# Performance work log

Measured on AMD Instinct MI355X. Metric: run time of the kernel, lower is better.

## Reference

```python
import jax, jax.numpy as jnp
import numpy as np
from jax import lax

RES = 2048
MAX_VAL = 1.0
COST_SCALE = 0.01
N_ITERS = 10
BOUNDARY_FRAC = 0.02  # sparse scattered Dirichlet cells, realistic for a planner occupancy grid


def _neighbor_sum(V):
    # replicate-pad (zero-Neumann at the outer border), 4-point stencil sum
    Vp = jnp.pad(V, 1, mode='edge')
    return Vp[:-2, 1:-1] + Vp[2:, 1:-1] + Vp[1:-1, :-2] + Vp[1:-1, 2:]


def setup_inputs() -> dict:
    key = jax.random.key(0)
    k1, k2, k3, k4 = jax.random.split(key, 4)
    x = jax.random.uniform(k1, (RES, RES), jnp.float32)
    # sparse boundary/obstacle cells (boundary_types > 0 means Dirichlet cell)
    boundary_types = (jax.random.uniform(k2, (RES, RES)) < BOUNDARY_FRAC).astype(jnp.int32)
    boundary_conditions = jax.random.uniform(k3, (RES, RES), jnp.float32)
    # learnable cost field, initialized around cost_scale (some negatives so ReLU matters)
    C = COST_SCALE + COST_SCALE * jax.random.normal(k4, (RES, RES), jnp.float32)
    return {'x': x, 'C': C, 'boundary_types': boundary_types,
            'boundary_conditions': boundary_conditions}


def reference(x, C, boundary_types, boundary_conditions):
    mask = boundary_types > 0
    # inject boundary conditions into the initial potential (x[obj_inds] = bc[obj_inds])
    V = jnp.where(mask, boundary_conditions, x)
    C_pos = jax.nn.relu(C)
    denom = 4.0 + C_pos  # screened Laplace: (4 + C) V = sum(neighbors)

    def step(V, _):
        V_new = _neighbor_sum(V) / denom
        V_new = jnp.where(mask, boundary_conditions, V_new)
        return V_new, None

    V, _ = lax.scan(step, V, None, length=N_ITERS)

    out = jnp.where(V >= MAX_VAL, 0.95 * MAX_VAL, V)
    out = jnp.where(mask, boundary_conditions, out)
    return out, C_pos
```

## Files before the change

kernel.cpp:

```cpp
#include <hip/hip_runtime.h>


#define RES    2048
#define HALO   10
#define DIMX   128
#define DIMY   56
#define OUTX   (DIMX - 2*HALO)
#define OUTY   (DIMY - 2*HALO)
#define NBX    ((RES + OUTX - 1) / OUTX)
#define NBY    ((RES + OUTY - 1) / OUTY)
#define NITER  10

__global__ __launch_bounds__(256, 2)
void laplace10_fused(const float* __restrict__ Xin,
                     const float* __restrict__ Cin,
                     const int*   __restrict__ BT,
                     const float* __restrict__ BCin,
                     float* __restrict__ OUT,
                     float* __restrict__ CPOS) {
  __shared__ __align__(16) float buf[2][DIMY][DIMX];
  float* const s0 = &buf[0][0][0];
  float* const s1 = &buf[1][0][0];

  const int t   = threadIdx.x;
  const int q   = t & 31;
  const int ty  = t >> 5;
  const int x0  = q * 4;
  const int y0  = ty * 7;
  const int tx0 = (int)blockIdx.x * OUTX - HALO;
  const int ty0 = (int)blockIdx.y * OUTY - HALO;
  const int gx0 = tx0 + x0;

  const bool xedge = (tx0 < 0) || (tx0 + DIMX > RES);

  auto stage = [&](const float* __restrict__ g, float* __restrict__ sb) {
    if (!xedge) {
#pragma unroll
      for (int i = 0; i < 14; ++i) {
        const int idx = t + i * 256;
        const int y   = idx >> 6;
        const int xx  = (idx & 63) * 2;
        int gy = ty0 + y;
        gy = gy < 0 ? 0 : (gy > RES - 1 ? RES - 1 : gy);
        *(float2*)(sb + y * DIMX + xx) =
            *(const float2*)(g + (size_t)gy * RES + (tx0 + xx));
      }
    } else {
#pragma unroll
      for (int i = 0; i < 14; ++i) {
        const int idx = t + i * 256;
        const int y   = idx >> 6;
        const int xx  = (idx & 63) * 2;
        int gy = ty0 + y;
        gy = gy < 0 ? 0 : (gy > RES - 1 ? RES - 1 : gy);
        int ga = tx0 + xx, gb = tx0 + xx + 1;
        ga = ga < 0 ? 0 : (ga > RES - 1 ? RES - 1 : ga);
        gb = gb < 0 ? 0 : (gb > RES - 1 ? RES - 1 : gb);
        float2 v;
        v.x = g[(size_t)gy * RES + ga];
        v.y = g[(size_t)gy * RES + gb];
        *(float2*)(sb + y * DIMX + xx) = v;
      }
    }
  };

  const bool in0 = (x0 + 0 >= HALO) && (x0 + 0 < HALO + OUTX);
  const bool in1 = (x0 + 1 >= HALO) && (x0 + 1 < HALO + OUTX);
  const bool in2 = (x0 + 2 >= HALO) && (x0 + 2 < HALO + OUTX);
  const bool in3 = (x0 + 3 >= HALO) && (x0 + 3 < HALO + OUTX);
  const bool fullq = in0 && in3 && (gx0 + 4 <= RES);

  stage((const float*)BT, s1);
  __syncthreads();
  unsigned mb = 0u;
#pragma unroll
  for (int i = 0; i < 7; ++i) {
    const float4 mv = *(const float4*)(s1 + (y0 + i) * DIMX + x0);
    if (__float_as_uint(mv.x) != 0u) mb |= 1u << (i * 4 + 0);
    if (__float_as_uint(mv.y) != 0u) mb |= 1u << (i * 4 + 1);
    if (__float_as_uint(mv.z) != 0u) mb |= 1u << (i * 4 + 2);
    if (__float_as_uint(mv.w) != 0u) mb |= 1u << (i * 4 + 3);
  }
  __syncthreads();

  stage(BCin, s1);
  __syncthreads();
  float4 Bq[7];
#pragma unroll
  for (int i = 0; i < 7; ++i) {
    const float4 b = *(const float4*)(s1 + (y0 + i) * DIMX + x0);
    Bq[i].x = (mb >> (i * 4 + 0) & 1u) ? b.x : 0.0f;
    Bq[i].y = (mb >> (i * 4 + 1) & 1u) ? b.y : 0.0f;
    Bq[i].z = (mb >> (i * 4 + 2) & 1u) ? b.z : 0.0f;
    Bq[i].w = (mb >> (i * 4 + 3) & 1u) ? b.w : 0.0f;
  }
  __syncthreads();

  stage(Cin, s1);
  __syncthreads();
  float4 Rq[7];
#pragma unroll
  for (int i = 0; i < 7; ++i) {
    const int y = y0 + i;
    const float4 c = *(const float4*)(s1 + y * DIMX + x0);
    float4 cp;
    cp.x = c.x > 0.0f ? c.x : 0.0f;
    cp.y = c.y > 0.0f ? c.y : 0.0f;
    cp.z = c.z > 0.0f ? c.z : 0.0f;
    cp.w = c.w > 0.0f ? c.w : 0.0f;
    Rq[i].x = (mb >> (i * 4 + 0) & 1u) ? 0.0f : 1.0f / (4.0f + cp.x);
    Rq[i].y = (mb >> (i * 4 + 1) & 1u) ? 0.0f : 1.0f / (4.0f + cp.y);
    Rq[i].z = (mb >> (i * 4 + 2) & 1u) ? 0.0f : 1.0f / (4.0f + cp.z);
    Rq[i].w = (mb >> (i * 4 + 3) & 1u) ? 0.0f : 1.0f / (4.0f + cp.w);
    const int gy = ty0 + y;
    if (y >= HALO && y < HALO + OUTY && gy < RES) {
      const size_t ro = (size_t)gy * RES;
      if (fullq) {
        *(float2*)(CPOS + ro + gx0)     = make_float2(cp.x, cp.y);
        *(float2*)(CPOS + ro + gx0 + 2) = make_float2(cp.z, cp.w);
      } else {
        if (in0 && gx0 + 0 < RES) CPOS[ro + gx0 + 0] = cp.x;
        if (in1 && gx0 + 1 < RES) CPOS[ro + gx0 + 1] = cp.y;
        if (in2 && gx0 + 2 < RES) CPOS[ro + gx0 + 2] = cp.z;
        if (in3 && gx0 + 3 < RES) CPOS[ro + gx0 + 3] = cp.w;
      }
    }
  }
  __syncthreads();

  stage(Xin, s1);
  __syncthreads();
#pragma unroll
  for (int i = 0; i < 7; ++i) {
    const float4 xv = *(const float4*)(s1 + (y0 + i) * DIMX + x0);
    float4 v0;
    v0.x = (mb >> (i * 4 + 0) & 1u) ? Bq[i].x : xv.x;
    v0.y = (mb >> (i * 4 + 1) & 1u) ? Bq[i].y : xv.y;
    v0.z = (mb >> (i * 4 + 2) & 1u) ? Bq[i].z : xv.z;
    v0.w = (mb >> (i * 4 + 3) & 1u) ? Bq[i].w : xv.w;
    *(float4*)(s0 + (y0 + i) * DIMX + x0) = v0;
  }
  __syncthreads();

  const int xm = (x0 == 0) ? 0 : x0 - 1;
  const int xp = (x0 + 4 >= DIMX) ? DIMX - 1 : x0 + 4;
  const bool lq0 = (gx0 + 0 <= 0);
  const bool lq1 = (gx0 + 1 <= 0);
  const bool lq2 = (gx0 + 2 <= 0);
  const bool lq3 = (gx0 + 3 <= 0);
  const bool rq0 = (gx0 + 0 >= RES - 1);
  const bool rq1 = (gx0 + 1 >= RES - 1);
  const bool rq2 = (gx0 + 2 >= RES - 1);
  const bool rq3 = (gx0 + 3 >= RES - 1);

#pragma unroll
  for (int it = 1; it <= NITER; ++it) {
    const float* const src = (it & 1) ? s0 : s1;
    float* const dst       = (it & 1) ? s1 : s0;
    float4 v[9];
#pragma unroll
    for (int j = 0; j < 9; ++j) {
      int r = y0 - 1 + j;
      r = r < 0 ? 0 : (r > DIMY - 1 ? DIMY - 1 : r);
      v[j] = *(const float4*)(src + r * DIMX + x0);
    }
#pragma unroll
    for (int i = 0; i < 7; ++i) {
      const int y = y0 + i;
      if (y < it || y >= DIMY - it) continue;
      const int gy = ty0 + y;
      const float lf = src[y * DIMX + xm];
      const float rt = src[y * DIMX + xp];
      const float4 vm = v[i + 1];
      const float4 va = (gy <= 0)       ? vm : v[i];
      const float4 vb = (gy >= RES - 1) ? vm : v[i + 2];
      const float n0 = va.x + vb.x + (lq0 ? vm.x : lf)   + (rq0 ? vm.x : vm.y);
      const float n1 = va.y + vb.y + (lq1 ? vm.y : vm.x) + (rq1 ? vm.y : vm.z);
      const float n2 = va.z + vb.z + (lq2 ? vm.z : vm.y) + (rq2 ? vm.z : vm.w);
      const float n3 = va.w + vb.w + (lq3 ? vm.w : vm.z) + (rq3 ? vm.w : rt);
      float4 nv;
      nv.x = fmaf(n0, Rq[i].x, Bq[i].x);
      nv.y = fmaf(n1, Rq[i].y, Bq[i].y);
      nv.z = fmaf(n2, Rq[i].z, Bq[i].z);
      nv.w = fmaf(n3, Rq[i].w, Bq[i].w);
      if (it < NITER) {
        *(float4*)(dst + y * DIMX + x0) = nv;
      } else {
        if (gy < RES) {
          const float o0 = (nv.x >= 1.0f) ? 0.95f : nv.x;
          const float o1 = (nv.y >= 1.0f) ? 0.95f : nv.y;
          const float o2 = (nv.z >= 1.0f) ? 0.95f : nv.z;
          const float o3 = (nv.w >= 1.0f) ? 0.95f : nv.w;
          const size_t ro = (size_t)gy * RES;
          if (fullq) {
            *(float2*)(OUT + ro + gx0)     = make_float2(o0, o1);
            *(float2*)(OUT + ro + gx0 + 2) = make_float2(o2, o3);
          } else {
            if (in0 && gx0 + 0 < RES) OUT[ro + gx0 + 0] = o0;
            if (in1 && gx0 + 1 < RES) OUT[ro + gx0 + 1] = o1;
            if (in2 && gx0 + 2 < RES) OUT[ro + gx0 + 2] = o2;
            if (in3 && gx0 + 3 < RES) OUT[ro + gx0 + 3] = o3;
          }
        }
      }
    }
    if (it < NITER) __syncthreads();
  }
}

extern "C" void kernel_launch(void* const* d_in, const int* in_sizes, int n_in,
                              void* d_out, int out_size, void* d_ws, size_t ws_size,
                              hipStream_t stream) {
  const float* Xin  = (const float*)d_in[0];
  const float* Cin  = (const float*)d_in[1];
  const int*   BT   = (const int*)d_in[2];
  const float* BCin = (const float*)d_in[3];
  float* OUT  = (float*)d_out;
  float* CPOS = OUT + (size_t)RES * RES;

  dim3 grid(NBX, NBY);
  dim3 block(256);
  hipLaunchKernelGGL(laplace10_fused, grid, block, 0, stream,
                     Xin, Cin, BT, BCin, OUT, CPOS);
}
```

Before: 152.0 us.

## Single-buffer LDS stencil with direct global loads, shuffles, and XCD-aware block remap

Replaces the double-buffered shared tile with one buffer updated in place between two barriers per iteration. Inputs are loaded straight from global memory into registers instead of being staged through shared memory. Left and right neighbours now come from wavefront shuffles rather than LDS reads. The launch becomes a 1D grid remapped so neighbouring tiles land on the same XCD, and the x halo grows to 12 so stores stay float4-aligned, with the occupancy hint raised to 4 blocks. Together these aim to cut LDS footprint and traffic and raise occupancy, at the cost of an extra barrier per iteration and more redundant halo work.

```diff
diff --git a/kernel.cpp b/kernel.cpp
--- a/kernel.cpp
+++ b/kernel.cpp
@@ -2,148 +2,53 @@
 
 
 #define RES    2048
-#define HALO   10
+#define XHALO  12
+#define YHALO  10
 #define DIMX   128
 #define DIMY   56
-#define OUTX   (DIMX - 2*HALO)
-#define OUTY   (DIMY - 2*HALO)
+#define OUTX   (DIMX - 2*XHALO)
+#define OUTY   (DIMY - 2*YHALO)
 #define NBX    ((RES + OUTX - 1) / OUTX)
 #define NBY    ((RES + OUTY - 1) / OUTY)
+#define NWG    (NBX*NBY)
 #define NITER  10
 
-__global__ __launch_bounds__(256, 2)
+__global__ __launch_bounds__(256, 4)
 void laplace10_fused(const float* __restrict__ Xin,
                      const float* __restrict__ Cin,
-                     const int*   __restrict__ BT,
+                     const float* __restrict__ BTf,
                      const float* __restrict__ BCin,
                      float* __restrict__ OUT,
                      float* __restrict__ CPOS) {
-  __shared__ __align__(16) float buf[2][DIMY][DIMX];
-  float* const s0 = &buf[0][0][0];
-  float* const s1 = &buf[1][0][0];
+  __shared__ __align__(16) float V[DIMY][DIMX];
 
-  const int t   = threadIdx.x;
-  const int q   = t & 31;
-  const int ty  = t >> 5;
-  const int x0  = q * 4;
-  const int y0  = ty * 7;
-  const int tx0 = (int)blockIdx.x * OUTX - HALO;
-  const int ty0 = (int)blockIdx.y * OUTY - HALO;
+  const int t  = threadIdx.x;
+  const int q  = t & 31;
+  const int ty = t >> 5;
+  const int x0 = q * 4;
+  const int y0 = ty * 7;
+
+  int wg = (int)blockIdx.x;
+  {
+    const int qq = NWG / 8, rr = NWG % 8;
+    const int xcd = wg % 8, off = wg / 8;
+    wg = (xcd < rr ? xcd * (qq + 1) : rr * (qq + 1) + (xcd - rr) * qq) + off;
+  }
+  const int bx  = wg % NBX, by = wg / NBX;
+  const int tx0 = bx * OUTX - XHALO;
+  const int ty0 = by * OUTY - YHALO;
   const int gx0 = tx0 + x0;
 
-  const bool xedge = (tx0 < 0) || (tx0 + DIMX > RES);
+  const bool xfull = (gx0 >= 0) && (gx0 + 4 <= RES);
+  const int  xcl   = (gx0 < 0) ? 0 : (RES - 1);
+  const bool xin   = (x0 >= XHALO) && (x0 < XHALO + OUTX) && xfull;
 
-  auto stage = [&](const float* __restrict__ g, float* __restrict__ sb) {
-    if (!xedge) {
-#pragma unroll
-      for (int i = 0; i < 14; ++i) {
-        const int idx = t + i * 256;
-        const int y   = idx >> 6;
-        const int xx  = (idx & 63) * 2;
-        int gy = ty0 + y;
-        gy = gy < 0 ? 0 : (gy > RES - 1 ? RES - 1 : gy);
-        *(float2*)(sb + y * DIMX + xx) =
-            *(const float2*)(g + (size_t)gy * RES + (tx0 + xx));
-      }
-    } else {
-#pragma unroll
-      for (int i = 0; i < 14; ++i) {
-        const int idx = t + i * 256;
-        const int y   = idx >> 6;
-        const int xx  = (idx & 63) * 2;
-        int gy = ty0 + y;
-        gy = gy < 0 ? 0 : (gy > RES - 1 ? RES - 1 : gy);
-        int ga = tx0 + xx, gb = tx0 + xx + 1;
-        ga = ga < 0 ? 0 : (ga > RES - 1 ? RES - 1 : ga);
-        gb = gb < 0 ? 0 : (gb > RES - 1 ? RES - 1 : gb);
-        float2 v;
-        v.x = g[(size_t)gy * RES + ga];
-        v.y = g[(size_t)gy * RES + gb];
-        *(float2*)(sb + y * DIMX + xx) = v;
-      }
-    }
+  auto load4 = [&](const float* __restrict__ g, int row) -> float4 {
+    if (xfull) return *(const float4*)(g + (size_t)row * RES + gx0);
+    const float v = g[(size_t)row * RES + xcl];
+    return make_float4(v, v, v, v);
   };
 
-  const bool in0 = (x0 + 0 >= HALO) && (x0 + 0 < HALO + OUTX);
-  const bool in1 = (x0 + 1 >= HALO) && (x0 + 1 < HALO + OUTX);
-  const bool in2 = (x0 + 2 >= HALO) && (x0 + 2 < HALO + OUTX);
-  const bool in3 = (x0 + 3 >= HALO) && (x0 + 3 < HALO + OUTX);
-  const bool fullq = in0 && in3 && (gx0 + 4 <= RES);
-
-  stage((const float*)BT, s1);
-  __syncthreads();
-  unsigned mb = 0u;
-#pragma unroll
-  for (int i = 0; i < 7; ++i) {
-    const float4 mv = *(const float4*)(s1 + (y0 + i) * DIMX + x0);
-    if (__float_as_uint(mv.x) != 0u) mb |= 1u << (i * 4 + 0);
-    if (__float_as_uint(mv.y) != 0u) mb |= 1u << (i * 4 + 1);
-    if (__float_as_uint(mv.z) != 0u) mb |= 1u << (i * 4 + 2);
-    if (__float_as_uint(mv.w) != 0u) mb |= 1u << (i * 4 + 3);
-  }
-  __syncthreads();
-
-  stage(BCin, s1);
-  __syncthreads();
-  float4 Bq[7];
-#pragma unroll
-  for (int i = 0; i < 7; ++i) {
-    const float4 b = *(const float4*)(s1 + (y0 + i) * DIMX + x0);
-    Bq[i].x = (mb >> (i * 4 + 0) & 1u) ? b.x : 0.0f;
-    Bq[i].y = (mb >> (i * 4 + 1) & 1u) ? b.y : 0.0f;
-    Bq[i].z = (mb >> (i * 4 + 2) & 1u) ? b.z : 0.0f;
-    Bq[i].w = (mb >> (i * 4 + 3) & 1u) ? b.w : 0.0f;
-  }
-  __syncthreads();
-
-  stage(Cin, s1);
-  __syncthreads();
-  float4 Rq[7];
-#pragma unroll
-  for (int i = 0; i < 7; ++i) {
-    const int y = y0 + i;
-    const float4 c = *(const float4*)(s1 + y * DIMX + x0);
-    float4 cp;
-    cp.x = c.x > 0.0f ? c.x : 0.0f;
-    cp.y = c.y > 0.0f ? c.y : 0.0f;
-    cp.z = c.z > 0.0f ? c.z : 0.0f;
-    cp.w = c.w > 0.0f ? c.w : 0.0f;
-    Rq[i].x = (mb >> (i * 4 + 0) & 1u) ? 0.0f : 1.0f / (4.0f + cp.x);
-    Rq[i].y = (mb >> (i * 4 + 1) & 1u) ? 0.0f : 1.0f / (4.0f + cp.y);
-    Rq[i].z = (mb >> (i * 4 + 2) & 1u) ? 0.0f : 1.0f / (4.0f + cp.z);
-    Rq[i].w = (mb >> (i * 4 + 3) & 1u) ? 0.0f : 1.0f / (4.0f + cp.w);
-    const int gy = ty0 + y;
-    if (y >= HALO && y < HALO + OUTY && gy < RES) {
-      const size_t ro = (size_t)gy * RES;
-      if (fullq) {
-        *(float2*)(CPOS + ro + gx0)     = make_float2(cp.x, cp.y);
-        *(float2*)(CPOS + ro + gx0 + 2) = make_float2(cp.z, cp.w);
-      } else {
-        if (in0 && gx0 + 0 < RES) CPOS[ro + gx0 + 0] = cp.x;
-        if (in1 && gx0 + 1 < RES) CPOS[ro + gx0 + 1] = cp.y;
-        if (in2 && gx0 + 2 < RES) CPOS[ro + gx0 + 2] = cp.z;
-        if (in3 && gx0 + 3 < RES) CPOS[ro + gx0 + 3] = cp.w;
-      }
-    }
-  }
-  __syncthreads();
-
-  stage(Xin, s1);
-  __syncthreads();
-#pragma unroll
-  for (int i = 0; i < 7; ++i) {
-    const float4 xv = *(const float4*)(s1 + (y0 + i) * DIMX + x0);
-    float4 v0;
-    v0.x = (mb >> (i * 4 + 0) & 1u) ? Bq[i].x : xv.x;
-    v0.y = (mb >> (i * 4 + 1) & 1u) ? Bq[i].y : xv.y;
-    v0.z = (mb >> (i * 4 + 2) & 1u) ? Bq[i].z : xv.z;
-    v0.w = (mb >> (i * 4 + 3) & 1u) ? Bq[i].w : xv.w;
-    *(float4*)(s0 + (y0 + i) * DIMX + x0) = v0;
-  }
-  __syncthreads();
-
-  const int xm = (x0 == 0) ? 0 : x0 - 1;
-  const int xp = (x0 + 4 >= DIMX) ? DIMX - 1 : x0 + 4;
   const bool lq0 = (gx0 + 0 <= 0);
   const bool lq1 = (gx0 + 1 <= 0);
   const bool lq2 = (gx0 + 2 <= 0);
@@ -153,58 +58,125 @@
   const bool rq2 = (gx0 + 2 >= RES - 1);
   const bool rq3 = (gx0 + 3 >= RES - 1);
 
+  unsigned mb = 0u;
+  float4 Bq[7], Rq[7];
 #pragma unroll
-  for (int it = 1; it <= NITER; ++it) {
-    const float* const src = (it & 1) ? s0 : s1;
-    float* const dst       = (it & 1) ? s1 : s0;
-    float4 v[9];
+  for (int i = 0; i < 7; ++i) {
+    const int gr  = ty0 + y0 + i;
+    const int gyc = gr < 0 ? 0 : (gr > RES - 1 ? RES - 1 : gr);
+    const float4 mv = load4(BTf, gyc);
+    const float4 bv = load4(BCin, gyc);
+    const unsigned m0 = (__float_as_uint(mv.x) != 0u);
+    const unsigned m1 = (__float_as_uint(mv.y) != 0u);
+    const unsigned m2 = (__float_as_uint(mv.z) != 0u);
+    const unsigned m3 = (__float_as_uint(mv.w) != 0u);
+    mb |= (m0 | (m1 << 1) | (m2 << 2) | (m3 << 3)) << (4 * i);
+    Bq[i].x = m0 ? bv.x : 0.0f;
+    Bq[i].y = m1 ? bv.y : 0.0f;
+    Bq[i].z = m2 ? bv.z : 0.0f;
+    Bq[i].w = m3 ? bv.w : 0.0f;
+  }
 #pragma unroll
-    for (int j = 0; j < 9; ++j) {
-      int r = y0 - 1 + j;
-      r = r < 0 ? 0 : (r > DIMY - 1 ? DIMY - 1 : r);
-      v[j] = *(const float4*)(src + r * DIMX + x0);
+  for (int i = 0; i < 7; ++i) {
+    const int gr  = ty0 + y0 + i;
+    const int gyc = gr < 0 ? 0 : (gr > RES - 1 ? RES - 1 : gr);
+    const float4 c = load4(Cin, gyc);
+    float4 cp;
+    cp.x = c.x > 0.0f ? c.x : 0.0f;
+    cp.y = c.y > 0.0f ? c.y : 0.0f;
+    cp.z = c.z > 0.0f ? c.z : 0.0f;
+    cp.w = c.w > 0.0f ? c.w : 0.0f;
+    Rq[i].x = (mb >> (4 * i + 0) & 1u) ? 0.0f : 1.0f / (4.0f + cp.x);
+    Rq[i].y = (mb >> (4 * i + 1) & 1u) ? 0.0f : 1.0f / (4.0f + cp.y);
+    Rq[i].z = (mb >> (4 * i + 2) & 1u) ? 0.0f : 1.0f / (4.0f + cp.z);
+    Rq[i].w = (mb >> (4 * i + 3) & 1u) ? 0.0f : 1.0f / (4.0f + cp.w);
+    const int yy = y0 + i;
+    if (xin && yy >= YHALO && yy < YHALO + OUTY && gr >= 0 && gr < RES) {
+      *(float4*)(CPOS + (size_t)gr * RES + gx0) = cp;
     }
+  }
+#pragma unroll
+  for (int i = 0; i < 7; ++i) {
+    const int gr  = ty0 + y0 + i;
+    const int gyc = gr < 0 ? 0 : (gr > RES - 1 ? RES - 1 : gr);
+    const float4 xv = load4(Xin, gyc);
+    float4 v0;
+    v0.x = (mb >> (4 * i + 0) & 1u) ? Bq[i].x : xv.x;
+    v0.y = (mb >> (4 * i + 1) & 1u) ? Bq[i].y : xv.y;
+    v0.z = (mb >> (4 * i + 2) & 1u) ? Bq[i].z : xv.z;
+    v0.w = (mb >> (4 * i + 3) & 1u) ? Bq[i].w : xv.w;
+    *(float4*)(&V[y0 + i][x0]) = v0;
+  }
+  __syncthreads();
+
+  auto compute_ns = [&](float4* ns) {
+    const int ym1 = (y0 == 0) ? 0 : y0 - 1;
+    float4 ra = *(const float4*)(&V[ym1][x0]);
+    float4 rb = *(const float4*)(&V[y0][x0]);
 #pragma unroll
     for (int i = 0; i < 7; ++i) {
-      const int y = y0 + i;
-      if (y < it || y >= DIMY - it) continue;
-      const int gy = ty0 + y;
-      const float lf = src[y * DIMX + xm];
-      const float rt = src[y * DIMX + xp];
-      const float4 vm = v[i + 1];
-      const float4 va = (gy <= 0)       ? vm : v[i];
-      const float4 vb = (gy >= RES - 1) ? vm : v[i + 2];
-      const float n0 = va.x + vb.x + (lq0 ? vm.x : lf)   + (rq0 ? vm.x : vm.y);
-      const float n1 = va.y + vb.y + (lq1 ? vm.y : vm.x) + (rq1 ? vm.y : vm.z);
-      const float n2 = va.z + vb.z + (lq2 ? vm.z : vm.y) + (rq2 ? vm.z : vm.w);
-      const float n3 = va.w + vb.w + (lq3 ? vm.w : vm.z) + (rq3 ? vm.w : rt);
-      float4 nv;
-      nv.x = fmaf(n0, Rq[i].x, Bq[i].x);
-      nv.y = fmaf(n1, Rq[i].y, Bq[i].y);
-      nv.z = fmaf(n2, Rq[i].z, Bq[i].z);
-      nv.w = fmaf(n3, Rq[i].w, Bq[i].w);
-      if (it < NITER) {
-        *(float4*)(dst + y * DIMX + x0) = nv;
-      } else {
-        if (gy < RES) {
-          const float o0 = (nv.x >= 1.0f) ? 0.95f : nv.x;
-          const float o1 = (nv.y >= 1.0f) ? 0.95f : nv.y;
-          const float o2 = (nv.z >= 1.0f) ? 0.95f : nv.z;
-          const float o3 = (nv.w >= 1.0f) ? 0.95f : nv.w;
-          const size_t ro = (size_t)gy * RES;
-          if (fullq) {
-            *(float2*)(OUT + ro + gx0)     = make_float2(o0, o1);
-            *(float2*)(OUT + ro + gx0 + 2) = make_float2(o2, o3);
-          } else {
-            if (in0 && gx0 + 0 < RES) OUT[ro + gx0 + 0] = o0;
-            if (in1 && gx0 + 1 < RES) OUT[ro + gx0 + 1] = o1;
-            if (in2 && gx0 + 2 < RES) OUT[ro + gx0 + 2] = o2;
-            if (in3 && gx0 + 3 < RES) OUT[ro + gx0 + 3] = o3;
-          }
+      const int yy = y0 + i;
+      const int yp = (yy >= DIMY - 1) ? (DIMY - 1) : (yy + 1);
+      const float4 rc = *(const float4*)(&V[yp][x0]);
+      const float lf = __shfl(rb.w, (t + 63) & 63);
+      const float rt = __shfl(rb.x, (t + 1) & 63);
+      const int g = ty0 + yy;
+      const float4 vm = rb;
+      const float4 va = (g <= 0) ? vm : ra;
+      const float4 vb = (g >= RES - 1) ? vm : rc;
+      float4 n;
+      n.x = va.x + vb.x + (lq0 ? vm.x : lf)   + (rq0 ? vm.x : vm.y);
+      n.y = va.y + vb.y + (lq1 ? vm.y : vm.x) + (rq1 ? vm.y : vm.z);
+      n.z = va.z + vb.z + (lq2 ? vm.z : vm.y) + (rq2 ? vm.z : vm.w);
+      n.w = va.w + vb.w + (lq3 ? vm.w : vm.z) + (rq3 ? vm.w : rt);
+      ns[i] = n;
+      ra = rb; rb = rc;
+    }
+  };
+
+#pragma unroll 1
+  for (int it = 1; it < NITER; ++it) {
+    float4 ns[7];
+    compute_ns(ns);
+    __syncthreads();
+#pragma unroll
+    for (int i = 0; i < 7; ++i) {
+      const int yy = y0 + i;
+      if (yy >= it && yy < DIMY - it) {
+        float4 nv;
+        nv.x = fmaf(ns[i].x, Rq[i].x, Bq[i].x);
+        nv.y = fmaf(ns[i].y, Rq[i].y, Bq[i].y);
+        nv.z = fmaf(ns[i].z, Rq[i].z, Bq[i].z);
+        nv.w = fmaf(ns[i].w, Rq[i].w, Bq[i].w);
+        *(float4*)(&V[yy][x0]) = nv;
+      }
+    }
+    __syncthreads();
+  }
+
+  {
+    float4 ns[7];
+    compute_ns(ns);
+#pragma unroll
+    for (int i = 0; i < 7; ++i) {
+      const int yy = y0 + i;
+      if (xin && yy >= YHALO && yy < YHALO + OUTY) {
+        const int g = ty0 + yy;
+        if (g < RES) {
+          float4 nv;
+          nv.x = fmaf(ns[i].x, Rq[i].x, Bq[i].x);
+          nv.y = fmaf(ns[i].y, Rq[i].y, Bq[i].y);
+          nv.z = fmaf(ns[i].z, Rq[i].z, Bq[i].z);
+          nv.w = fmaf(ns[i].w, Rq[i].w, Bq[i].w);
+          float4 o;
+          o.x = (nv.x >= 1.0f) ? 0.95f : nv.x;
+          o.y = (nv.y >= 1.0f) ? 0.95f : nv.y;
+          o.z = (nv.z >= 1.0f) ? 0.95f : nv.z;
+          o.w = (nv.w >= 1.0f) ? 0.95f : nv.w;
+          *(float4*)(OUT + (size_t)g * RES + gx0) = o;
         }
       }
     }
-    if (it < NITER) __syncthreads();
   }
 }
 
@@ -213,13 +185,11 @@
                               hipStream_t stream) {
   const float* Xin  = (const float*)d_in[0];
   const float* Cin  = (const float*)d_in[1];
-  const int*   BT   = (const int*)d_in[2];
+  const float* BTf  = (const float*)d_in[2];
   const float* BCin = (const float*)d_in[3];
   float* OUT  = (float*)d_out;
   float* CPOS = OUT + (size_t)RES * RES;
 
-  dim3 grid(NBX, NBY);
-  dim3 block(256);
-  hipLaunchKernelGGL(laplace10_fused, grid, block, 0, stream,
-                     Xin, Cin, BT, BCin, OUT, CPOS);
+  hipLaunchKernelGGL(laplace10_fused, dim3(NWG), dim3(256), 0, stream,
+                     Xin, Cin, BTf, BCin, OUT, CPOS);
 }
```

New measurement: 153.8 us. Within noise of the previous version (+1.2%).
